# Optimization experiments

Hardware: AMD Instinct MI355X
Metric: run time of the kernel (lower is better)

The kernel has to match this reference:

```python
import jax, jax.numpy as jnp
import numpy as np

D = 1024          # in_features == out_features
RATIO = 2         # mlp_ratio
E = 4             # num_experts
H = D * RATIO     # proj1 output width
HH = H // 2       # max SwiGLU half-width
N = 16384         # tokens (batch*seq flattened)


def setup_inputs() -> dict:
    key = jax.random.key(0)
    k = jax.random.split(key, 6)
    x = jax.random.normal(k[0], (N, D), dtype=jnp.float32)
    expert_mask = jax.random.randint(k[1], (N,), 0, E)
    s1 = 1.0 / np.sqrt(D)
    w1 = jax.random.uniform(k[2], (H, D), jnp.float32, -s1, s1)
    b1 = jax.random.uniform(k[3], (H,), jnp.float32, -s1, s1)
    s2 = 1.0 / np.sqrt(H)
    w2 = jax.random.uniform(k[4], (D, H), jnp.float32, -s2, s2)
    b2 = jax.random.uniform(k[5], (D,), jnp.float32, -s2, s2)
    return {"x": x, "w1": w1, "b1": b1, "w2": w2, "b2": b2, "expert_mask": expert_mask}


def reference(x, w1, b1, w2, b2, expert_mask):
    # nested dim per token: expert e -> d_e = D / 2^(E-1-e); largest expert uses full D
    d_tok = D // (2 ** (E - 1 - expert_mask))          # [N] int
    h_half = (RATIO * d_tok) // 2                       # SwiGLU half-width per token

    # nested expand: only first d_e input dims participate
    xm = jnp.where(jnp.arange(D)[None, :] < d_tok[:, None], x, 0.0)
    h = xm @ w1.T + b1                                  # [N, H]; only [:, :h_e] is valid per token

    hid = jnp.arange(HH)
    gate_mask = hid[None, :] < h_half[:, None]          # [N, HH]
    gate = jnp.where(gate_mask, h[:, :HH], 0.0)         # gate = h[:h_half]
    up = jnp.take_along_axis(h, h_half[:, None] + hid[None, :], axis=1)  # up = h[h_half:2*h_half]
    act = jnp.where(gate_mask, jax.nn.silu(gate) * up, 0.0)             # [N, HH]

    # nested contract: only first h_half columns of w2 and first d_e output dims
    out = act @ w2[:, :HH].T + b2                       # [N, D]
    out = jnp.where(jnp.arange(D)[None, :] < d_tok[:, None], out, 0.0)
    return out
```

## Files before the change

### kernel.cpp

```cpp
#include <hip/hip_runtime.h>
#include <math.h>
#include <stdint.h>


#define NTOK 16384
#define DDIM 1024
#define HDIM 2048

typedef unsigned short u16;
typedef __attribute__((ext_vector_type(8))) short short8;
typedef __attribute__((ext_vector_type(4))) float f32x4;

__device__ __forceinline__ u16 f2bf(float f) {
    uint32_t u = __float_as_uint(f);
    return (u16)((u + 0x7fffu + ((u >> 16) & 1u)) >> 16);
}
__device__ __forceinline__ float bf2f(u16 h) {
    return __uint_as_float(((uint32_t)h) << 16);
}
__device__ __forceinline__ void split8(const float* __restrict__ src,
                                       u16* __restrict__ dsth, u16* __restrict__ dstl) {
    float4 v0 = *(const float4*)(src);
    float4 v1 = *(const float4*)(src + 4);
    float t[8] = {v0.x, v0.y, v0.z, v0.w, v1.x, v1.y, v1.z, v1.w};
    short8 h8, l8;
#pragma unroll
    for (int i = 0; i < 8; ++i) {
        u16 h = f2bf(t[i]);
        u16 l = f2bf(t[i] - bf2f(h));
        h8[i] = (short)h;
        l8[i] = (short)l;
    }
    *(short8*)dsth = h8;
    *(short8*)dstl = l8;
}

__device__ __forceinline__ void gload16(const void* g, void* l) {
    __builtin_amdgcn_global_load_lds(
        (const __attribute__((address_space(1))) void*)g,
        (__attribute__((address_space(3))) void*)l,
        16, 0, 0);
}

__global__ __launch_bounds__(64) void k_zero(int* __restrict__ counts) {
    if (threadIdx.x < 4) counts[threadIdx.x] = 0;
}

__global__ __launch_bounds__(256) void k_bin(const int* __restrict__ mask,
                                             int* __restrict__ counts,
                                             int* __restrict__ bucket) {
    int i = blockIdx.x * 256 + threadIdx.x;
    int e = mask[i];
    int pos = atomicAdd(&counts[e], 1);
    bucket[e * NTOK + pos] = i;
}

__global__ __launch_bounds__(256) void k_wsplit(const float* __restrict__ w1,
                                                const float* __restrict__ w2,
                                                u16* __restrict__ w1h, u16* __restrict__ w1l,
                                                u16* __restrict__ w2h, u16* __restrict__ w2l) {
    size_t o = ((size_t)blockIdx.x * 256 + threadIdx.x) * 8;
    split8(&w1[o], &w1h[o], &w1l[o]);
    split8(&w2[o], &w2h[o], &w2l[o]);
}

__global__ __launch_bounds__(256) void k_xsplit(const float* __restrict__ x,
                                                u16* __restrict__ xh, u16* __restrict__ xl) {
    size_t o = ((size_t)blockIdx.x * 256 + threadIdx.x) * 8;
    split8(&x[o], &xh[o], &xl[o]);
}

template <int DE>
__device__ void phaseA_v3(const u16* __restrict__ xh, const u16* __restrict__ xl,
                          const u16* __restrict__ w1h, const u16* __restrict__ w1l,
                          const float* __restrict__ b1,
                          const int* __restrict__ bucket, int cnt, int jt,
                          u16* __restrict__ acth, u16* __restrict__ actl,
                          int* toks, u16* lds) {
    const int tid = threadIdx.x;
    const int lane = tid & 63;
    const int wid = tid >> 6;
    const int wr = wid >> 1, wc = wid & 1;
    const int j0 = jt * 64;
    const int lr = lane & 15;
    const int lgrp = lane >> 4;
    const int nk = DE / 32;

    for (int tile = blockIdx.x; tile * 64 < cnt; tile += gridDim.x) {
        const int base = tile * 64;
        __syncthreads();
        if (tid < 64) {
            int p = base + tid;
            toks[tid] = bucket[p < cnt ? p : cnt - 1];
        }
        __syncthreads();

        const u16* src[6];
        int dstoff[6];
        {
            const int r16 = lane >> 2, pc = lane & 3;
#pragma unroll
            for (int q = 0; q < 6; ++q) {
                int idx = wid * 6 + q;
                int a = idx >> 2, p = idx & 3;
                int r = p * 16 + r16;
                int ko = (pc ^ ((r >> 1) & 3)) * 8;
                const u16* s;
                if (a == 0)      s = &xh[(size_t)toks[r] * DDIM + ko];
                else if (a == 1) s = &xl[(size_t)toks[r] * DDIM + ko];
                else if (a == 2) s = &w1h[(size_t)(j0 + r) * DDIM + ko];
                else if (a == 3) s = &w1l[(size_t)(j0 + r) * DDIM + ko];
                else if (a == 4) s = &w1h[(size_t)(DE + j0 + r) * DDIM + ko];
                else             s = &w1l[(size_t)(DE + j0 + r) * DDIM + ko];
                src[q] = s;
                dstoff[q] = a * 2048 + p * 512;
            }
        }

        f32x4 gacc[2][2], uacc[2][2];
        const f32x4 zz = {0.f, 0.f, 0.f, 0.f};
#pragma unroll
        for (int mi = 0; mi < 2; ++mi)
#pragma unroll
            for (int ni = 0; ni < 2; ++ni) { gacc[mi][ni] = zz; uacc[mi][ni] = zz; }

#pragma unroll
        for (int q = 0; q < 6; ++q) gload16(src[q], lds + dstoff[q]);
        __syncthreads();

        for (int kt = 0; kt < nk; ++kt) {
            const int cur = kt & 1;
            if (kt + 1 < nk) {
                const int boff = (cur ^ 1) * 12288;
                const int kc = (kt + 1) * 32;
#pragma unroll
                for (int q = 0; q < 6; ++q) gload16(src[q] + kc, lds + boff + dstoff[q]);
            }
            const u16* B = lds + cur * 12288;
            short8 Ah[2], Al[2];
#pragma unroll
            for (int mi = 0; mi < 2; ++mi) {
                int row = wr * 32 + mi * 16 + lr;
                int pb = (lgrp ^ ((row >> 1) & 3)) * 8;
                Ah[mi] = *(const short8*)&B[0 * 2048 + row * 32 + pb];
                Al[mi] = *(const short8*)&B[1 * 2048 + row * 32 + pb];
            }
#pragma unroll
            for (int ni = 0; ni < 2; ++ni) {
                int rowb = wc * 32 + ni * 16 + lr;
                int pb = (lgrp ^ ((rowb >> 1) & 3)) * 8;
                short8 bgh = *(const short8*)&B[2 * 2048 + rowb * 32 + pb];
                short8 bgl = *(const short8*)&B[3 * 2048 + rowb * 32 + pb];
                short8 buh = *(const short8*)&B[4 * 2048 + rowb * 32 + pb];
                short8 bul = *(const short8*)&B[5 * 2048 + rowb * 32 + pb];
#pragma unroll
                for (int mi = 0; mi < 2; ++mi) {
                    gacc[mi][ni] = __builtin_amdgcn_mfma_f32_16x16x32_bf16(Ah[mi], bgh, gacc[mi][ni], 0, 0, 0);
                    gacc[mi][ni] = __builtin_amdgcn_mfma_f32_16x16x32_bf16(Ah[mi], bgl, gacc[mi][ni], 0, 0, 0);
                    gacc[mi][ni] = __builtin_amdgcn_mfma_f32_16x16x32_bf16(Al[mi], bgh, gacc[mi][ni], 0, 0, 0);
                    uacc[mi][ni] = __builtin_amdgcn_mfma_f32_16x16x32_bf16(Ah[mi], buh, uacc[mi][ni], 0, 0, 0);
                    uacc[mi][ni] = __builtin_amdgcn_mfma_f32_16x16x32_bf16(Ah[mi], bul, uacc[mi][ni], 0, 0, 0);
                    uacc[mi][ni] = __builtin_amdgcn_mfma_f32_16x16x32_bf16(Al[mi], buh, uacc[mi][ni], 0, 0, 0);
                }
            }
            __syncthreads();
        }

#pragma unroll
        for (int ni = 0; ni < 2; ++ni) {
            int gcol = j0 + wc * 32 + ni * 16 + lr;
            float bg = b1[gcol];
            float bu = b1[DE + gcol];
#pragma unroll
            for (int mi = 0; mi < 2; ++mi) {
#pragma unroll
                for (int r = 0; r < 4; ++r) {
                    int trow = wr * 32 + mi * 16 + lgrp * 4 + r;
                    if (base + trow < cnt) {
                        float g = gacc[mi][ni][r] + bg;
                        float u = uacc[mi][ni][r] + bu;
                        float a = (g / (1.0f + expf(-g))) * u;
                        size_t off = (size_t)toks[trow] * DDIM + gcol;
                        u16 h = f2bf(a);
                        acth[off] = h;
                        actl[off] = f2bf(a - bf2f(h));
                    }
                }
            }
        }
    }
}

__global__ __launch_bounds__(256) void k_phaseA_v3(const u16* __restrict__ xh,
                                                   const u16* __restrict__ xl,
                                                   const u16* __restrict__ w1h,
                                                   const u16* __restrict__ w1l,
                                                   const float* __restrict__ b1,
                                                   const int* __restrict__ counts,
                                                   const int* __restrict__ bucket,
                                                   u16* __restrict__ acth,
                                                   u16* __restrict__ actl) {
    __shared__ int toks[64];
    __shared__ __align__(16) u16 lds[2 * 6 * 2048];
    int y = blockIdx.y;
    if (y < 2)
        phaseA_v3<128>(xh, xl, w1h, w1l, b1, bucket + 0 * NTOK, counts[0], y, acth, actl, toks, lds);
    else if (y < 6)
        phaseA_v3<256>(xh, xl, w1h, w1l, b1, bucket + 1 * NTOK, counts[1], y - 2, acth, actl, toks, lds);
    else if (y < 14)
        phaseA_v3<512>(xh, xl, w1h, w1l, b1, bucket + 2 * NTOK, counts[2], y - 6, acth, actl, toks, lds);
    else
        phaseA_v3<1024>(xh, xl, w1h, w1l, b1, bucket + 3 * NTOK, counts[3], y - 14, acth, actl, toks, lds);
}

template <int DE>
__device__ void phaseB_v3(const u16* __restrict__ acth, const u16* __restrict__ actl,
                          const u16* __restrict__ w2h, const u16* __restrict__ w2l,
                          const float* __restrict__ b2,
                          const int* __restrict__ bucket, int cnt, int it,
                          float* __restrict__ out,
                          int* toks, u16* lds) {
    const int tid = threadIdx.x;
    const int lane = tid & 63;
    const int wid = tid >> 6;
    const int wr = wid >> 1, wc = wid & 1;
    const int i0 = it * 64;
    const int lr = lane & 15;
    const int lgrp = lane >> 4;
    const int nk = DE / 32;

    for (int tile = blockIdx.x; tile * 64 < cnt; tile += gridDim.x) {
        const int base = tile * 64;
        __syncthreads();
        if (tid < 64) {
            int p = base + tid;
            toks[tid] = bucket[p < cnt ? p : cnt - 1];
        }
        __syncthreads();

        const u16* src[4];
        int dstoff[4];
        {
            const int r16 = lane >> 2, pc = lane & 3;
#pragma unroll
            for (int q = 0; q < 4; ++q) {
                int idx = wid * 4 + q;
                int a = idx >> 2, p = idx & 3;
                int r = p * 16 + r16;
                int ko = (pc ^ ((r >> 1) & 3)) * 8;
                const u16* s;
                if (a == 0)      s = &acth[(size_t)toks[r] * DDIM + ko];
                else if (a == 1) s = &actl[(size_t)toks[r] * DDIM + ko];
                else if (a == 2) s = &w2h[(size_t)(i0 + r) * HDIM + ko];
                else             s = &w2l[(size_t)(i0 + r) * HDIM + ko];
                src[q] = s;
                dstoff[q] = a * 2048 + p * 512;
            }
        }

        f32x4 acc[2][2];
        const f32x4 zz = {0.f, 0.f, 0.f, 0.f};
#pragma unroll
        for (int mi = 0; mi < 2; ++mi)
#pragma unroll
            for (int ni = 0; ni < 2; ++ni) acc[mi][ni] = zz;

#pragma unroll
        for (int q = 0; q < 4; ++q) gload16(src[q], lds + dstoff[q]);
        __syncthreads();

        for (int kt = 0; kt < nk; ++kt) {
            const int cur = kt & 1;
            if (kt + 1 < nk) {
                const int boff = (cur ^ 1) * 8192;
                const int kc = (kt + 1) * 32;
#pragma unroll
                for (int q = 0; q < 4; ++q) gload16(src[q] + kc, lds + boff + dstoff[q]);
            }
            const u16* B = lds + cur * 8192;
            short8 Ah[2], Al[2];
#pragma unroll
            for (int mi = 0; mi < 2; ++mi) {
                int row = wr * 32 + mi * 16 + lr;
                int pb = (lgrp ^ ((row >> 1) & 3)) * 8;
                Ah[mi] = *(const short8*)&B[0 * 2048 + row * 32 + pb];
                Al[mi] = *(const short8*)&B[1 * 2048 + row * 32 + pb];
            }
#pragma unroll
            for (int ni = 0; ni < 2; ++ni) {
                int rowb = wc * 32 + ni * 16 + lr;
                int pb = (lgrp ^ ((rowb >> 1) & 3)) * 8;
                short8 bh = *(const short8*)&B[2 * 2048 + rowb * 32 + pb];
                short8 bl = *(const short8*)&B[3 * 2048 + rowb * 32 + pb];
#pragma unroll
                for (int mi = 0; mi < 2; ++mi) {
                    acc[mi][ni] = __builtin_amdgcn_mfma_f32_16x16x32_bf16(Ah[mi], bh, acc[mi][ni], 0, 0, 0);
                    acc[mi][ni] = __builtin_amdgcn_mfma_f32_16x16x32_bf16(Ah[mi], bl, acc[mi][ni], 0, 0, 0);
                    acc[mi][ni] = __builtin_amdgcn_mfma_f32_16x16x32_bf16(Al[mi], bh, acc[mi][ni], 0, 0, 0);
                }
            }
            __syncthreads();
        }

#pragma unroll
        for (int ni = 0; ni < 2; ++ni) {
            int icol = i0 + wc * 32 + ni * 16 + lr;
            float bb = b2[icol];
#pragma unroll
            for (int mi = 0; mi < 2; ++mi) {
#pragma unroll
                for (int r = 0; r < 4; ++r) {
                    int trow = wr * 32 + mi * 16 + lgrp * 4 + r;
                    if (base + trow < cnt)
                        out[(size_t)toks[trow] * DDIM + icol] = acc[mi][ni][r] + bb;
                }
            }
        }

        if (it == 0 && DE < DDIM) {
            constexpr int TAIL4 = (DDIM - DE) / 4;
            const float4 z{0.f, 0.f, 0.f, 0.f};
            for (int idx = tid; idx < 64 * TAIL4; idx += 256) {
                int r = idx / TAIL4, c = idx % TAIL4;
                if (base + r < cnt)
                    *(float4*)&out[(size_t)toks[r] * DDIM + DE + c * 4] = z;
            }
        }
    }
}

__global__ __launch_bounds__(256) void k_phaseB_v3(const u16* __restrict__ acth,
                                                   const u16* __restrict__ actl,
                                                   const u16* __restrict__ w2h,
                                                   const u16* __restrict__ w2l,
                                                   const float* __restrict__ b2,
                                                   const int* __restrict__ counts,
                                                   const int* __restrict__ bucket,
                                                   float* __restrict__ out) {
    __shared__ int toks[64];
    __shared__ __align__(16) u16 lds[2 * 4 * 2048];
    int y = blockIdx.y;
    if (y < 2)
        phaseB_v3<128>(acth, actl, w2h, w2l, b2, bucket + 0 * NTOK, counts[0], y, out, toks, lds);
    else if (y < 6)
        phaseB_v3<256>(acth, actl, w2h, w2l, b2, bucket + 1 * NTOK, counts[1], y - 2, out, toks, lds);
    else if (y < 14)
        phaseB_v3<512>(acth, actl, w2h, w2l, b2, bucket + 2 * NTOK, counts[2], y - 6, out, toks, lds);
    else
        phaseB_v3<1024>(acth, actl, w2h, w2l, b2, bucket + 3 * NTOK, counts[3], y - 14, out, toks, lds);
}

template <int DE>
__device__ void phaseA_impl(const float* __restrict__ x, const float* __restrict__ w1,
                            const float* __restrict__ b1, const int* __restrict__ bucket,
                            int cnt, int jt, float* __restrict__ actout, int tileIdx,
                            int* toks, float* Xs, float* Wg, float* Wu) {
    constexpr int BT = 64, BJ = 64, KC = 32, KP = 36;
    const int tid = threadIdx.x;
    const int base = tileIdx * BT;
    if (base >= cnt) return;
    if (tid < BT) {
        int p = base + tid;
        toks[tid] = bucket[p < cnt ? p : cnt - 1];
    }
    __syncthreads();
    const int tg = tid & 15;
    const int cg = tid >> 4;
    const int j0 = jt * BJ;
    float ag[4][4] = {};
    float au[4][4] = {};
    for (int kc = 0; kc < DE; kc += KC) {
        for (int idx = tid; idx < BT * (KC / 4); idx += 256) {
            int r = idx >> 3, jf = idx & 7;
            *(float4*)&Xs[r * KP + jf * 4] = *(const float4*)&x[(size_t)toks[r] * DDIM + kc + jf * 4];
        }
        for (int idx = tid; idx < BJ * (KC / 4); idx += 256) {
            int r = idx >> 3, jf = idx & 7;
            *(float4*)&Wg[r * KP + jf * 4] = *(const float4*)&w1[(size_t)(j0 + r) * DDIM + kc + jf * 4];
            *(float4*)&Wu[r * KP + jf * 4] = *(const float4*)&w1[(size_t)(DE + j0 + r) * DDIM + kc + jf * 4];
        }
        __syncthreads();
#pragma unroll
        for (int k4 = 0; k4 < KC / 4; ++k4) {
            float4 xv[4];
#pragma unroll
            for (int tt = 0; tt < 4; ++tt) xv[tt] = *(const float4*)&Xs[(tg + 16 * tt) * KP + k4 * 4];
#pragma unroll
            for (int c = 0; c < 4; ++c) {
                float4 wg = *(const float4*)&Wg[(cg * 4 + c) * KP + k4 * 4];
                float4 wu = *(const float4*)&Wu[(cg * 4 + c) * KP + k4 * 4];
#pragma unroll
                for (int tt = 0; tt < 4; ++tt) {
                    float s = ag[tt][c];
                    s = fmaf(xv[tt].x, wg.x, s); s = fmaf(xv[tt].y, wg.y, s);
                    s = fmaf(xv[tt].z, wg.z, s); s = fmaf(xv[tt].w, wg.w, s);
                    ag[tt][c] = s;
                    float t2 = au[tt][c];
                    t2 = fmaf(xv[tt].x, wu.x, t2); t2 = fmaf(xv[tt].y, wu.y, t2);
                    t2 = fmaf(xv[tt].z, wu.z, t2); t2 = fmaf(xv[tt].w, wu.w, t2);
                    au[tt][c] = t2;
                }
            }
        }
        __syncthreads();
    }
    float4 bg = *(const float4*)&b1[j0 + cg * 4];
    float4 bu = *(const float4*)&b1[DE + j0 + cg * 4];
#pragma unroll
    for (int tt = 0; tt < 4; ++tt) {
        int tl = tg + 16 * tt;
        if (base + tl < cnt) {
            float g0 = ag[tt][0] + bg.x, g1 = ag[tt][1] + bg.y;
            float g2 = ag[tt][2] + bg.z, g3 = ag[tt][3] + bg.w;
            float u0 = au[tt][0] + bu.x, u1 = au[tt][1] + bu.y;
            float u2 = au[tt][2] + bu.z, u3 = au[tt][3] + bu.w;
            float4 o;
            o.x = (g0 / (1.0f + expf(-g0))) * u0;
            o.y = (g1 / (1.0f + expf(-g1))) * u1;
            o.z = (g2 / (1.0f + expf(-g2))) * u2;
            o.w = (g3 / (1.0f + expf(-g3))) * u3;
            *(float4*)&actout[(size_t)toks[tl] * DDIM + j0 + cg * 4] = o;
        }
    }
}

__global__ __launch_bounds__(256) void k_phaseA(const float* __restrict__ x,
                                                const float* __restrict__ w1,
                                                const float* __restrict__ b1,
                                                const int* __restrict__ counts,
                                                const int* __restrict__ bucket,
                                                float* __restrict__ out) {
    __shared__ int toks[64];
    __shared__ __align__(16) float Xs[64 * 36];
    __shared__ __align__(16) float Wg[64 * 36];
    __shared__ __align__(16) float Wu[64 * 36];
    int y = blockIdx.y;
    if (y < 2)
        phaseA_impl<128>(x, w1, b1, bucket + 0 * NTOK, counts[0], y, out, blockIdx.x, toks, Xs, Wg, Wu);
    else if (y < 6)
        phaseA_impl<256>(x, w1, b1, bucket + 1 * NTOK, counts[1], y - 2, out, blockIdx.x, toks, Xs, Wg, Wu);
    else if (y < 14)
        phaseA_impl<512>(x, w1, b1, bucket + 2 * NTOK, counts[2], y - 6, out, blockIdx.x, toks, Xs, Wg, Wu);
    else
        phaseA_impl<1024>(x, w1, b1, bucket + 3 * NTOK, counts[3], y - 14, out, blockIdx.x, toks, Xs, Wg, Wu);
}

template <int DE, int BT, int NI>
__device__ void phaseB_impl(const float* __restrict__ w2, const float* __restrict__ b2,
                            const int* __restrict__ bucket, int cnt, float* __restrict__ out,
                            int tileIdx, int* toks, float* As, float* Wt) {
    constexpr int KC = 16;
    constexpr int DEP = DE + 4;
    constexpr int NIP = NI + 4;
    constexpr int CT = 4;
    constexpr int CG = NI / CT;
    constexpr int TG = 256 / CG;
    static_assert(BT / TG == 4, "thread token tile must be 4");
    const int tid = threadIdx.x;
    const int base = tileIdx * BT;
    if (base >= cnt) return;
    if (tid < BT) {
        int p = base + tid;
        toks[tid] = bucket[p < cnt ? p : cnt - 1];
    }
    __syncthreads();
    for (int idx = tid; idx < BT * (DE / 4); idx += 256) {
        int r = idx / (DE / 4), jf = idx % (DE / 4);
        *(float4*)&As[r * DEP + jf * 4] = *(const float4*)&out[(size_t)toks[r] * DDIM + jf * 4];
    }
    __syncthreads();
    const int tg = tid % TG;
    const int cg = tid / TG;
    for (int i0 = 0; i0 < DE; i0 += NI) {
        float acc[4][4] = {};
        for (int jc = 0; jc < DE; jc += KC) {
            __syncthreads();
            for (int idx = tid; idx < NI * (KC / 4); idx += 256) {
                int i = idx >> 2, jf4 = idx & 3;
                float4 v = *(const float4*)&w2[(size_t)(i0 + i) * HDIM + jc + jf4 * 4];
                Wt[(jf4 * 4 + 0) * NIP + i] = v.x;
                Wt[(jf4 * 4 + 1) * NIP + i] = v.y;
                Wt[(jf4 * 4 + 2) * NIP + i] = v.z;
                Wt[(jf4 * 4 + 3) * NIP + i] = v.w;
            }
            __syncthreads();
#pragma unroll
            for (int j4 = 0; j4 < KC / 4; ++j4) {
                float xr[4][4];
#pragma unroll
                for (int tt = 0; tt < 4; ++tt) {
                    float4 v = *(const float4*)&As[(tg + TG * tt) * DEP + jc + j4 * 4];
                    xr[tt][0] = v.x; xr[tt][1] = v.y; xr[tt][2] = v.z; xr[tt][3] = v.w;
                }
#pragma unroll
                for (int jj = 0; jj < 4; ++jj) {
                    float4 wv = *(const float4*)&Wt[(j4 * 4 + jj) * NIP + cg * CT];
#pragma unroll
                    for (int tt = 0; tt < 4; ++tt) {
                        float xs = xr[tt][jj];
                        acc[tt][0] = fmaf(xs, wv.x, acc[tt][0]);
                        acc[tt][1] = fmaf(xs, wv.y, acc[tt][1]);
                        acc[tt][2] = fmaf(xs, wv.z, acc[tt][2]);
                        acc[tt][3] = fmaf(xs, wv.w, acc[tt][3]);
                    }
                }
            }
        }
        float4 bb = *(const float4*)&b2[i0 + cg * CT];
#pragma unroll
        for (int tt = 0; tt < 4; ++tt) {
            int tl = tg + TG * tt;
            if (base + tl < cnt) {
                float4 o;
                o.x = acc[tt][0] + bb.x;
                o.y = acc[tt][1] + bb.y;
                o.z = acc[tt][2] + bb.z;
                o.w = acc[tt][3] + bb.w;
                *(float4*)&out[(size_t)toks[tl] * DDIM + i0 + cg * CT] = o;
            }
        }
    }
    if (DE < DDIM) {
        constexpr int TAIL4 = (DDIM - DE) / 4;
        float4 z{0.f, 0.f, 0.f, 0.f};
        for (int idx = tid; idx < BT * TAIL4; idx += 256) {
            int r = idx / TAIL4, jf = idx % TAIL4;
            if (base + r < cnt)
                *(float4*)&out[(size_t)toks[r] * DDIM + DE + jf * 4] = z;
        }
    }
}

__global__ __launch_bounds__(256) void k_phaseB(const float* __restrict__ w2,
                                                const float* __restrict__ b2,
                                                const int* __restrict__ counts,
                                                const int* __restrict__ bucket,
                                                float* __restrict__ out) {
    __shared__ int toks[64];
    __shared__ __align__(16) float As[8448];
    __shared__ __align__(16) float Wt[8256];
    switch (blockIdx.y) {
        case 0: phaseB_impl<128, 64, 64>(w2, b2, bucket + 0 * NTOK, counts[0], out, blockIdx.x, toks, As, Wt); break;
        case 1: phaseB_impl<256, 32, 128>(w2, b2, bucket + 1 * NTOK, counts[1], out, blockIdx.x, toks, As, Wt); break;
        case 2: phaseB_impl<512, 16, 256>(w2, b2, bucket + 2 * NTOK, counts[2], out, blockIdx.x, toks, As, Wt); break;
        case 3: phaseB_impl<1024, 8, 512>(w2, b2, bucket + 3 * NTOK, counts[3], out, blockIdx.x, toks, As, Wt); break;
    }
}

extern "C" void kernel_launch(void* const* d_in, const int* in_sizes, int n_in,
                              void* d_out, int out_size, void* d_ws, size_t ws_size,
                              hipStream_t stream) {
    const float* x  = (const float*)d_in[0];
    const float* w1 = (const float*)d_in[1];
    const float* b1 = (const float*)d_in[2];
    const float* w2 = (const float*)d_in[3];
    const float* b2 = (const float*)d_in[4];
    const int* mask = (const int*)d_in[5];
    float* out = (float*)d_out;

    char* wsb = (char*)d_ws;
    int* counts = (int*)wsb;
    int* bucket = (int*)(wsb + 256);
    u16* acth = (u16*)(wsb + 262400);
    u16* actl = (u16*)(wsb + 33816832);
    u16* w1h = (u16*)(wsb + 67371264);
    u16* w1l = (u16*)(wsb + 71565568);
    u16* w2h = (u16*)(wsb + 75759872);
    u16* w2l = (u16*)(wsb + 79954176);
    const size_t NEED = 84148480ull;

    hipLaunchKernelGGL(k_zero, dim3(1), dim3(64), 0, stream, counts);
    hipLaunchKernelGGL(k_bin, dim3(NTOK / 256), dim3(256), 0, stream, mask, counts, bucket);

    if (ws_size >= NEED) {
        u16* xh = (u16*)d_out;
        u16* xl = xh + (size_t)NTOK * DDIM;
        hipLaunchKernelGGL(k_wsplit, dim3(1024), dim3(256), 0, stream, w1, w2, w1h, w1l, w2h, w2l);
        hipLaunchKernelGGL(k_xsplit, dim3(8192), dim3(256), 0, stream, x, xh, xl);
        hipLaunchKernelGGL(k_phaseA_v3, dim3(64, 30), dim3(256), 0, stream,
                           xh, xl, w1h, w1l, b1, counts, bucket, acth, actl);
        hipLaunchKernelGGL(k_phaseB_v3, dim3(64, 30), dim3(256), 0, stream,
                           acth, actl, w2h, w2l, b2, counts, bucket, out);
    } else {
        hipLaunchKernelGGL(k_phaseA, dim3(NTOK / 64, 30), dim3(256), 0, stream, x, w1, b1, counts, bucket, out);
        hipLaunchKernelGGL(k_phaseB, dim3(NTOK / 8, 4), dim3(256), 0, stream, w2, b2, counts, bucket, out);
    }
}
```

Measured before the change: 456.9 us.

## Triple-buffer LDS GEMM pipeline with vmcnt waits and block-local binning

Both MFMA GEMM phases move from double-buffered LDS staging with full __syncthreads to a three-stage ring. Loads are issued two k-steps ahead, and explicit s_waitcnt vmcnt plus raw s_barrier let global-to-LDS copies overlap more compute. The binning kernel now ranks tokens with LDS atomics and issues one global atomic per expert per block, cutting global atomic contention. The fallback FP32 path is removed, which makes the large workspace mandatory, and LDS use per block grows, which may lower occupancy.

```diff
diff --git a/kernel.cpp b/kernel.cpp
--- a/kernel.cpp
+++ b/kernel.cpp
@@ -49,10 +49,17 @@
 __global__ __launch_bounds__(256) void k_bin(const int* __restrict__ mask,
                                              int* __restrict__ counts,
                                              int* __restrict__ bucket) {
-    int i = blockIdx.x * 256 + threadIdx.x;
-    int e = mask[i];
-    int pos = atomicAdd(&counts[e], 1);
-    bucket[e * NTOK + pos] = i;
+    __shared__ int lcnt[4], lbase[4];
+    const int tid = threadIdx.x;
+    const int i = blockIdx.x * 256 + tid;
+    if (tid < 4) lcnt[tid] = 0;
+    __syncthreads();
+    const int e = mask[i];
+    const int rank = atomicAdd(&lcnt[e], 1);
+    __syncthreads();
+    if (tid < 4) lbase[tid] = atomicAdd(&counts[tid], lcnt[tid]);
+    __syncthreads();
+    bucket[e * NTOK + lbase[e] + rank] = i;
 }
 
 __global__ __launch_bounds__(256) void k_wsplit(const float* __restrict__ w1,
@@ -85,6 +92,7 @@
     const int lr = lane & 15;
     const int lgrp = lane >> 4;
     const int nk = DE / 32;
+    constexpr int BUF = 12288;
 
     for (int tile = blockIdx.x; tile * 64 < cnt; tile += gridDim.x) {
         const int base = tile * 64;
@@ -126,17 +134,26 @@
 
 #pragma unroll
         for (int q = 0; q < 6; ++q) gload16(src[q], lds + dstoff[q]);
-        __syncthreads();
-
+#pragma unroll
+        for (int q = 0; q < 6; ++q) gload16(src[q] + 32, lds + BUF + dstoff[q]);
+
+        int coff = 0;
+        int soff = 2 * BUF;
         for (int kt = 0; kt < nk; ++kt) {
-            const int cur = kt & 1;
-            if (kt + 1 < nk) {
-                const int boff = (cur ^ 1) * 12288;
-                const int kc = (kt + 1) * 32;
-#pragma unroll
-                for (int q = 0; q < 6; ++q) gload16(src[q] + kc, lds + boff + dstoff[q]);
-            }
-            const u16* B = lds + cur * 12288;
+            if (kt + 2 < nk) {
+                const int kc = (kt + 2) * 32;
+#pragma unroll
+                for (int q = 0; q < 6; ++q) gload16(src[q] + kc, lds + soff + dstoff[q]);
+                asm volatile("s_waitcnt vmcnt(12)" ::: "memory");
+            } else if (kt + 1 < nk) {
+                asm volatile("s_waitcnt vmcnt(6)" ::: "memory");
+            } else {
+                asm volatile("s_waitcnt vmcnt(0)" ::: "memory");
+            }
+            __builtin_amdgcn_s_barrier();
+            __builtin_amdgcn_sched_barrier(0);
+
+            const u16* B = lds + coff;
             short8 Ah[2], Al[2];
 #pragma unroll
             for (int mi = 0; mi < 2; ++mi) {
@@ -163,7 +180,11 @@
                     uacc[mi][ni] = __builtin_amdgcn_mfma_f32_16x16x32_bf16(Al[mi], buh, uacc[mi][ni], 0, 0, 0);
                 }
             }
-            __syncthreads();
+            __builtin_amdgcn_sched_barrier(0);
+            __builtin_amdgcn_s_barrier();
+
+            coff = (coff == 2 * BUF) ? 0 : coff + BUF;
+            soff = (soff == 2 * BUF) ? 0 : soff + BUF;
         }
 
 #pragma unroll
@@ -201,7 +222,7 @@
                                                    u16* __restrict__ acth,
                                                    u16* __restrict__ actl) {
     __shared__ int toks[64];
-    __shared__ __align__(16) u16 lds[2 * 6 * 2048];
+    __shared__ __align__(16) u16 lds[3 * 6 * 2048];
     int y = blockIdx.y;
     if (y < 2)
         phaseA_v3<128>(xh, xl, w1h, w1l, b1, bucket + 0 * NTOK, counts[0], y, acth, actl, toks, lds);
@@ -228,6 +249,7 @@
     const int lr = lane & 15;
     const int lgrp = lane >> 4;
     const int nk = DE / 32;
+    constexpr int BUF = 8192;
 
     for (int tile = blockIdx.x; tile * 64 < cnt; tile += gridDim.x) {
         const int base = tile * 64;
@@ -267,17 +289,26 @@
 
 #pragma unroll
         for (int q = 0; q < 4; ++q) gload16(src[q], lds + dstoff[q]);
-        __syncthreads();
-
+#pragma unroll
+        for (int q = 0; q < 4; ++q) gload16(src[q] + 32, lds + BUF + dstoff[q]);
+
+        int coff = 0;
+        int soff = 2 * BUF;
         for (int kt = 0; kt < nk; ++kt) {
-            const int cur = kt & 1;
-            if (kt + 1 < nk) {
-                const int boff = (cur ^ 1) * 8192;
-                const int kc = (kt + 1) * 32;
-#pragma unroll
-                for (int q = 0; q < 4; ++q) gload16(src[q] + kc, lds + boff + dstoff[q]);
-            }
-            const u16* B = lds + cur * 8192;
+            if (kt + 2 < nk) {
+                const int kc = (kt + 2) * 32;
+#pragma unroll
+                for (int q = 0; q < 4; ++q) gload16(src[q] + kc, lds + soff + dstoff[q]);
+                asm volatile("s_waitcnt vmcnt(8)" ::: "memory");
+            } else if (kt + 1 < nk) {
+                asm volatile("s_waitcnt vmcnt(4)" ::: "memory");
+            } else {
+                asm volatile("s_waitcnt vmcnt(0)" ::: "memory");
+            }
+            __builtin_amdgcn_s_barrier();
+            __builtin_amdgcn_sched_barrier(0);
+
+            const u16* B = lds + coff;
             short8 Ah[2], Al[2];
 #pragma unroll
             for (int mi = 0; mi < 2; ++mi) {
@@ -299,7 +330,11 @@
                     acc[mi][ni] = __builtin_amdgcn_mfma_f32_16x16x32_bf16(Al[mi], bh, acc[mi][ni], 0, 0, 0);
                 }
             }
-            __syncthreads();
+            __builtin_amdgcn_sched_barrier(0);
+            __builtin_amdgcn_s_barrier();
+
+            coff = (coff == 2 * BUF) ? 0 : coff + BUF;
+            soff = (soff == 2 * BUF) ? 0 : soff + BUF;
         }
 
 #pragma unroll
@@ -338,7 +373,7 @@
                                                    const int* __restrict__ bucket,
                                                    float* __restrict__ out) {
     __shared__ int toks[64];
-    __shared__ __align__(16) u16 lds[2 * 4 * 2048];
+    __shared__ __align__(16) u16 lds[3 * 4 * 2048];
     int y = blockIdx.y;
     if (y < 2)
         phaseB_v3<128>(acth, actl, w2h, w2l, b2, bucket + 0 * NTOK, counts[0], y, out, toks, lds);
@@ -348,203 +383,6 @@
         phaseB_v3<512>(acth, actl, w2h, w2l, b2, bucket + 2 * NTOK, counts[2], y - 6, out, toks, lds);
     else
         phaseB_v3<1024>(acth, actl, w2h, w2l, b2, bucket + 3 * NTOK, counts[3], y - 14, out, toks, lds);
-}
-
-template <int DE>
-__device__ void phaseA_impl(const float* __restrict__ x, const float* __restrict__ w1,
-                            const float* __restrict__ b1, const int* __restrict__ bucket,
-                            int cnt, int jt, float* __restrict__ actout, int tileIdx,
-                            int* toks, float* Xs, float* Wg, float* Wu) {
-    constexpr int BT = 64, BJ = 64, KC = 32, KP = 36;
-    const int tid = threadIdx.x;
-    const int base = tileIdx * BT;
-    if (base >= cnt) return;
-    if (tid < BT) {
-        int p = base + tid;
-        toks[tid] = bucket[p < cnt ? p : cnt - 1];
-    }
-    __syncthreads();
-    const int tg = tid & 15;
-    const int cg = tid >> 4;
-    const int j0 = jt * BJ;
-    float ag[4][4] = {};
-    float au[4][4] = {};
-    for (int kc = 0; kc < DE; kc += KC) {
-        for (int idx = tid; idx < BT * (KC / 4); idx += 256) {
-            int r = idx >> 3, jf = idx & 7;
-            *(float4*)&Xs[r * KP + jf * 4] = *(const float4*)&x[(size_t)toks[r] * DDIM + kc + jf * 4];
-        }
-        for (int idx = tid; idx < BJ * (KC / 4); idx += 256) {
-            int r = idx >> 3, jf = idx & 7;
-            *(float4*)&Wg[r * KP + jf * 4] = *(const float4*)&w1[(size_t)(j0 + r) * DDIM + kc + jf * 4];
-            *(float4*)&Wu[r * KP + jf * 4] = *(const float4*)&w1[(size_t)(DE + j0 + r) * DDIM + kc + jf * 4];
-        }
-        __syncthreads();
-#pragma unroll
-        for (int k4 = 0; k4 < KC / 4; ++k4) {
-            float4 xv[4];
-#pragma unroll
-            for (int tt = 0; tt < 4; ++tt) xv[tt] = *(const float4*)&Xs[(tg + 16 * tt) * KP + k4 * 4];
-#pragma unroll
-            for (int c = 0; c < 4; ++c) {
-                float4 wg = *(const float4*)&Wg[(cg * 4 + c) * KP + k4 * 4];
-                float4 wu = *(const float4*)&Wu[(cg * 4 + c) * KP + k4 * 4];
-#pragma unroll
-                for (int tt = 0; tt < 4; ++tt) {
-                    float s = ag[tt][c];
-                    s = fmaf(xv[tt].x, wg.x, s); s = fmaf(xv[tt].y, wg.y, s);
-                    s = fmaf(xv[tt].z, wg.z, s); s = fmaf(xv[tt].w, wg.w, s);
-                    ag[tt][c] = s;
-                    float t2 = au[tt][c];
-                    t2 = fmaf(xv[tt].x, wu.x, t2); t2 = fmaf(xv[tt].y, wu.y, t2);
-                    t2 = fmaf(xv[tt].z, wu.z, t2); t2 = fmaf(xv[tt].w, wu.w, t2);
-                    au[tt][c] = t2;
-                }
-            }
-        }
-        __syncthreads();
-    }
-    float4 bg = *(const float4*)&b1[j0 + cg * 4];
-    float4 bu = *(const float4*)&b1[DE + j0 + cg * 4];
-#pragma unroll
-    for (int tt = 0; tt < 4; ++tt) {
-        int tl = tg + 16 * tt;
-        if (base + tl < cnt) {
-            float g0 = ag[tt][0] + bg.x, g1 = ag[tt][1] + bg.y;
-            float g2 = ag[tt][2] + bg.z, g3 = ag[tt][3] + bg.w;
-            float u0 = au[tt][0] + bu.x, u1 = au[tt][1] + bu.y;
-            float u2 = au[tt][2] + bu.z, u3 = au[tt][3] + bu.w;
-            float4 o;
-            o.x = (g0 / (1.0f + expf(-g0))) * u0;
-            o.y = (g1 / (1.0f + expf(-g1))) * u1;
-            o.z = (g2 / (1.0f + expf(-g2))) * u2;
-            o.w = (g3 / (1.0f + expf(-g3))) * u3;
-            *(float4*)&actout[(size_t)toks[tl] * DDIM + j0 + cg * 4] = o;
-        }
-    }
-}
-
-__global__ __launch_bounds__(256) void k_phaseA(const float* __restrict__ x,
-                                                const float* __restrict__ w1,
-                                                const float* __restrict__ b1,
-                                                const int* __restrict__ counts,
-                                                const int* __restrict__ bucket,
-                                                float* __restrict__ out) {
-    __shared__ int toks[64];
-    __shared__ __align__(16) float Xs[64 * 36];
-    __shared__ __align__(16) float Wg[64 * 36];
-    __shared__ __align__(16) float Wu[64 * 36];
-    int y = blockIdx.y;
-    if (y < 2)
-        phaseA_impl<128>(x, w1, b1, bucket + 0 * NTOK, counts[0], y, out, blockIdx.x, toks, Xs, Wg, Wu);
-    else if (y < 6)
-        phaseA_impl<256>(x, w1, b1, bucket + 1 * NTOK, counts[1], y - 2, out, blockIdx.x, toks, Xs, Wg, Wu);
-    else if (y < 14)
-        phaseA_impl<512>(x, w1, b1, bucket + 2 * NTOK, counts[2], y - 6, out, blockIdx.x, toks, Xs, Wg, Wu);
-    else
-        phaseA_impl<1024>(x, w1, b1, bucket + 3 * NTOK, counts[3], y - 14, out, blockIdx.x, toks, Xs, Wg, Wu);
-}
-
-template <int DE, int BT, int NI>
-__device__ void phaseB_impl(const float* __restrict__ w2, const float* __restrict__ b2,
-                            const int* __restrict__ bucket, int cnt, float* __restrict__ out,
-                            int tileIdx, int* toks, float* As, float* Wt) {
-    constexpr int KC = 16;
-    constexpr int DEP = DE + 4;
-    constexpr int NIP = NI + 4;
-    constexpr int CT = 4;
-    constexpr int CG = NI / CT;
-    constexpr int TG = 256 / CG;
-    static_assert(BT / TG == 4, "thread token tile must be 4");
-    const int tid = threadIdx.x;
-    const int base = tileIdx * BT;
-    if (base >= cnt) return;
-    if (tid < BT) {
-        int p = base + tid;
-        toks[tid] = bucket[p < cnt ? p : cnt - 1];
-    }
-    __syncthreads();
-    for (int idx = tid; idx < BT * (DE / 4); idx += 256) {
-        int r = idx / (DE / 4), jf = idx % (DE / 4);
-        *(float4*)&As[r * DEP + jf * 4] = *(const float4*)&out[(size_t)toks[r] * DDIM + jf * 4];
-    }
-    __syncthreads();
-    const int tg = tid % TG;
-    const int cg = tid / TG;
-    for (int i0 = 0; i0 < DE; i0 += NI) {
-        float acc[4][4] = {};
-        for (int jc = 0; jc < DE; jc += KC) {
-            __syncthreads();
-            for (int idx = tid; idx < NI * (KC / 4); idx += 256) {
-                int i = idx >> 2, jf4 = idx & 3;
-                float4 v = *(const float4*)&w2[(size_t)(i0 + i) * HDIM + jc + jf4 * 4];
-                Wt[(jf4 * 4 + 0) * NIP + i] = v.x;
-                Wt[(jf4 * 4 + 1) * NIP + i] = v.y;
-                Wt[(jf4 * 4 + 2) * NIP + i] = v.z;
-                Wt[(jf4 * 4 + 3) * NIP + i] = v.w;
-            }
-            __syncthreads();
-#pragma unroll
-            for (int j4 = 0; j4 < KC / 4; ++j4) {
-                float xr[4][4];
-#pragma unroll
-                for (int tt = 0; tt < 4; ++tt) {
-                    float4 v = *(const float4*)&As[(tg + TG * tt) * DEP + jc + j4 * 4];
-                    xr[tt][0] = v.x; xr[tt][1] = v.y; xr[tt][2] = v.z; xr[tt][3] = v.w;
-                }
-#pragma unroll
-                for (int jj = 0; jj < 4; ++jj) {
-                    float4 wv = *(const float4*)&Wt[(j4 * 4 + jj) * NIP + cg * CT];
-#pragma unroll
-                    for (int tt = 0; tt < 4; ++tt) {
-                        float xs = xr[tt][jj];
-                        acc[tt][0] = fmaf(xs, wv.x, acc[tt][0]);
-                        acc[tt][1] = fmaf(xs, wv.y, acc[tt][1]);
-                        acc[tt][2] = fmaf(xs, wv.z, acc[tt][2]);
-                        acc[tt][3] = fmaf(xs, wv.w, acc[tt][3]);
-                    }
-                }
-            }
-        }
-        float4 bb = *(const float4*)&b2[i0 + cg * CT];
-#pragma unroll
-        for (int tt = 0; tt < 4; ++tt) {
-            int tl = tg + TG * tt;
-            if (base + tl < cnt) {
-                float4 o;
-                o.x = acc[tt][0] + bb.x;
-                o.y = acc[tt][1] + bb.y;
-                o.z = acc[tt][2] + bb.z;
-                o.w = acc[tt][3] + bb.w;
-                *(float4*)&out[(size_t)toks[tl] * DDIM + i0 + cg * CT] = o;
-            }
-        }
-    }
-    if (DE < DDIM) {
-        constexpr int TAIL4 = (DDIM - DE) / 4;
-        float4 z{0.f, 0.f, 0.f, 0.f};
-        for (int idx = tid; idx < BT * TAIL4; idx += 256) {
-            int r = idx / TAIL4, jf = idx % TAIL4;
-            if (base + r < cnt)
-                *(float4*)&out[(size_t)toks[r] * DDIM + DE + jf * 4] = z;
-        }
-    }
-}
-
-__global__ __launch_bounds__(256) void k_phaseB(const float* __restrict__ w2,
-                                                const float* __restrict__ b2,
-                                                const int* __restrict__ counts,
-                                                const int* __restrict__ bucket,
-                                                float* __restrict__ out) {
-    __shared__ int toks[64];
-    __shared__ __align__(16) float As[8448];
-    __shared__ __align__(16) float Wt[8256];
-    switch (blockIdx.y) {
-        case 0: phaseB_impl<128, 64, 64>(w2, b2, bucket + 0 * NTOK, counts[0], out, blockIdx.x, toks, As, Wt); break;
-        case 1: phaseB_impl<256, 32, 128>(w2, b2, bucket + 1 * NTOK, counts[1], out, blockIdx.x, toks, As, Wt); break;
-        case 2: phaseB_impl<512, 16, 256>(w2, b2, bucket + 2 * NTOK, counts[2], out, blockIdx.x, toks, As, Wt); break;
-        case 3: phaseB_impl<1024, 8, 512>(w2, b2, bucket + 3 * NTOK, counts[3], out, blockIdx.x, toks, As, Wt); break;
-    }
 }
 
 extern "C" void kernel_launch(void* const* d_in, const int* in_sizes, int n_in,
@@ -567,22 +405,16 @@
     u16* w1l = (u16*)(wsb + 71565568);
     u16* w2h = (u16*)(wsb + 75759872);
     u16* w2l = (u16*)(wsb + 79954176);
-    const size_t NEED = 84148480ull;
 
     hipLaunchKernelGGL(k_zero, dim3(1), dim3(64), 0, stream, counts);
     hipLaunchKernelGGL(k_bin, dim3(NTOK / 256), dim3(256), 0, stream, mask, counts, bucket);
 
-    if (ws_size >= NEED) {
-        u16* xh = (u16*)d_out;
-        u16* xl = xh + (size_t)NTOK * DDIM;
-        hipLaunchKernelGGL(k_wsplit, dim3(1024), dim3(256), 0, stream, w1, w2, w1h, w1l, w2h, w2l);
-        hipLaunchKernelGGL(k_xsplit, dim3(8192), dim3(256), 0, stream, x, xh, xl);
-        hipLaunchKernelGGL(k_phaseA_v3, dim3(64, 30), dim3(256), 0, stream,
-                           xh, xl, w1h, w1l, b1, counts, bucket, acth, actl);
-        hipLaunchKernelGGL(k_phaseB_v3, dim3(64, 30), dim3(256), 0, stream,
-                           acth, actl, w2h, w2l, b2, counts, bucket, out);
-    } else {
-        hipLaunchKernelGGL(k_phaseA, dim3(NTOK / 64, 30), dim3(256), 0, stream, x, w1, b1, counts, bucket, out);
-        hipLaunchKernelGGL(k_phaseB, dim3(NTOK / 8, 4), dim3(256), 0, stream, w2, b2, counts, bucket, out);
-    }
-}
+    u16* xh = (u16*)d_out;
+    u16* xl = xh + (size_t)NTOK * DDIM;
+    hipLaunchKernelGGL(k_wsplit, dim3(1024), dim3(256), 0, stream, w1, w2, w1h, w1l, w2h, w2l);
+    hipLaunchKernelGGL(k_xsplit, dim3(8192), dim3(256), 0, stream, x, xh, xl);
+    hipLaunchKernelGGL(k_phaseA_v3, dim3(64, 30), dim3(256), 0, stream,
+                       xh, xl, w1h, w1l, b1, counts, bucket, acth, actl);
+    hipLaunchKernelGGL(k_phaseB_v3, dim3(64, 30), dim3(256), 0, stream,
+                       acth, actl, w2h, w2l, b2, counts, bucket, out);
+}
```

New measurement: 384.2 us. 1.19x faster.
